# Optimization experiments

Hardware: AMD Instinct MI355X
Metric: run time of the kernel (lower is better)

The kernel has to match this reference:

```python
import jax, jax.numpy as jnp
import numpy as np

B, S, T = 512, 1024, 48

def setup_inputs() -> dict:
    key = jax.random.key(0)
    k1, k2, k3, k4, k5 = jax.random.split(key, 5)
    emissions = jax.random.normal(k1, (B, S, T), dtype=jnp.float32)
    tags = jax.random.randint(k2, (B, S), 0, T, dtype=jnp.int32)
    mask = jnp.ones((B, S), dtype=jnp.float32)
    transitions = jax.random.normal(k3, (T, T), dtype=jnp.float32)
    start_transitions = jax.random.normal(k4, (T,), dtype=jnp.float32)
    end_transitions = jax.random.normal(k5, (T,), dtype=jnp.float32)
    return {"emissions": emissions, "tags": tags, "mask": mask,
            "transitions": transitions, "start_transitions": start_transitions,
            "end_transitions": end_transitions}

def _crf_loss(emissions, transitions, start_transitions, end_transitions, tags, mask):
    # ---- numerator: score of the gold path (fully vectorized over seq) ----
    emit = jnp.take_along_axis(emissions, tags[..., None], axis=2)[..., 0]  # (B,S)
    trans = transitions[tags[:, 1:], tags[:, :-1]]                          # (B,S-1)
    lengths = jnp.sum(mask, axis=1).astype(jnp.int32)
    last_idx = jnp.clip(lengths - 1, 0)
    last_tags = jnp.take_along_axis(tags, last_idx[:, None], axis=1)[:, 0]
    numerator = (start_transitions[tags[:, 0]] + emit[:, 0]
                 + jnp.sum(mask[:, 1:] * (emit[:, 1:] + trans), axis=1)
                 + end_transitions[last_tags])                               # (B,)

    # ---- denominator: log-partition via forward algorithm (lax.scan) ----
    def step(score, x):
        em_i, m_i = x  # (B,T), (B,)
        # logsumexp over previous tag; emission is prev-independent so add outside
        nxt = jax.nn.logsumexp(score[:, :, None] + transitions.T[None, :, :], axis=1) + em_i
        score = jnp.where(m_i[:, None] > 0, nxt, score)
        return score, None

    init = start_transitions[None, :] + emissions[:, 0]                      # (B,T)
    xs = (jnp.swapaxes(emissions[:, 1:], 0, 1), jnp.swapaxes(mask[:, 1:], 0, 1))
    final, _ = jax.lax.scan(step, init, xs)
    denominator = jax.nn.logsumexp(final + end_transitions[None, :], axis=1)  # (B,)

    return jnp.mean(denominator - numerator)

def reference(emissions, tags, mask, transitions, start_transitions, end_transitions):
    return _crf_loss(emissions, transitions, start_transitions, end_transitions, tags, mask)
```

## Files before the change

kernel.cpp:

```cpp
#include <hip/hip_runtime.h>
#include <math.h>

#define Bn 512
#define Sn 1024
#define Tn 48
#define NSEG 16
#define SEGLEN 64

typedef _Float16 h2 __attribute__((ext_vector_type(2)));
typedef _Float16 h4 __attribute__((ext_vector_type(4)));
typedef float    f4 __attribute__((ext_vector_type(4)));

static constexpr float LOG2E = 1.4426950408889634f;
static constexpr float LN2f  = 0.6931471805599453f;

#define MFMA16(A, B, C) __builtin_amdgcn_mfma_f32_16x16x16f16((A), (B), (C), 0, 0, 0)

__device__ __forceinline__ h2 hmax2(h2 a, h2 b) {
#if __has_builtin(__builtin_elementwise_max)
  return __builtin_elementwise_max(a, b);
#else
  h2 r;
  r[0] = a[0] > b[0] ? a[0] : b[0];
  r[1] = a[1] > b[1] ? a[1] : b[1];
  return r;
#endif
}
__device__ __forceinline__ h2 cvt2(float a, float b) {
  return __builtin_bit_cast(h2, __builtin_amdgcn_cvt_pkrtz(a, b));
}
__device__ __forceinline__ h4 mkh4(h2 lo, h2 hi) {
  return __builtin_shufflevector(lo, hi, 0, 1, 2, 3);
}
__device__ __forceinline__ h2 loh(h4 v) { return __builtin_shufflevector(v, v, 0, 1); }
__device__ __forceinline__ h2 hih(h4 v) { return __builtin_shufflevector(v, v, 2, 3); }

__global__ __launch_bounds__(256) void ehgen(const float* __restrict__ em,
                                             _Float16* __restrict__ out) {
  const size_t total = (size_t)Bn * Sn * Tn;
  const size_t i = ((size_t)blockIdx.x * 256 + threadIdx.x) * 8;
  if (i >= total) return;
  const f4 a = *(const f4*)(em + i);
  const f4 b = *(const f4*)(em + i + 4);
  h4 o1, o2;
  #pragma unroll
  for (int j = 0; j < 4; ++j) {
    o1[j] = (_Float16)__builtin_amdgcn_exp2f(fmaf(a[j], LOG2E, -6.0f));
    o2[j] = (_Float16)__builtin_amdgcn_exp2f(fmaf(b[j], LOG2E, -6.0f));
  }
  *(h4*)(out + i) = o1;
  *(h4*)(out + i + 4) = o2;
}

template <bool PRE>
__global__ __launch_bounds__(1024, 2)
void crf_fwd_seg(const float* __restrict__ em,
                 const float* __restrict__ mask,
                 const float* __restrict__ trans,
                 const float* __restrict__ startt,
                 const float* __restrict__ endt,
                 const _Float16* __restrict__ eh16,
                 float* __restrict__ den_out)
{
  const int b   = blockIdx.x;
  const int tid = threadIdx.x;
  const int wid = tid >> 6;
  const int l   = tid & 63;
  const int c16 = l & 15;
  const int g   = l >> 4;

  __shared__ float lwbuf[64];

  const float*    __restrict__ emb = em + (size_t)b * Sn * Tn;
  const float*    __restrict__ mkb = mask + (size_t)b * Sn;
  const _Float16* __restrict__ ehL = PRE ? (eh16 + (size_t)b * Sn * Tn + 4 * g) : nullptr;
  const float*    __restrict__ emL = emb + 4 * g;

  h4 Afr[3][3];
  float mtg;
  {
    float tl[3][3][4];
    float mt = -1e30f;
    #pragma unroll
    for (int rt = 0; rt < 3; ++rt)
      #pragma unroll
      for (int kt = 0; kt < 3; ++kt) {
        const f4 t4 = *(const f4*)(trans + (16 * rt + c16) * Tn + 16 * kt + 4 * g);
        #pragma unroll
        for (int i = 0; i < 4; ++i) {
          const float v = t4[i] * LOG2E;
          tl[rt][kt][i] = v;
          mt = fmaxf(mt, v);
        }
      }
    #pragma unroll
    for (int off = 1; off < 64; off <<= 1) mt = fmaxf(mt, __shfl_xor(mt, off));
    mtg = mt;
    #pragma unroll
    for (int rt = 0; rt < 3; ++rt)
      #pragma unroll
      for (int kt = 0; kt < 3; ++kt) {
        h4 r;
        #pragma unroll
        for (int i = 0; i < 4; ++i)
          r[i] = (_Float16)__builtin_amdgcn_exp2f(tl[rt][kt][i] - mtg);
        Afr[rt][kt] = r;
      }
  }

  h4 Bfr[3][3];
  float Mc[3] = {0.f, 0.f, 0.f};
  float cnt = 0.f;
  #pragma unroll
  for (int kt = 0; kt < 3; ++kt)
    #pragma unroll
    for (int ct = 0; ct < 3; ++ct) {
      h4 r;
      #pragma unroll
      for (int i = 0; i < 4; ++i)
        r[i] = (_Float16)(((16 * kt + 4 * g + i) == (16 * ct + c16)) ? 1.0f : 0.0f);
      Bfr[kt][ct] = r;
    }

  auto STEP = [&](const h4& e0, const h4& e1, const h4& e2, float mkval,
                  bool APPLY, const float (&scv)[3], const float (&shv)[3]) {
    if (__int_as_float(__builtin_amdgcn_readfirstlane(__float_as_int(mkval))) > 0.0f) {
      f4 acc[3][3];
      #pragma unroll
      for (int rt = 0; rt < 3; ++rt)
        #pragma unroll
        for (int ct = 0; ct < 3; ++ct) acc[rt][ct] = f4{0.f, 0.f, 0.f, 0.f};
      #pragma unroll
      for (int kt = 0; kt < 3; ++kt)
        #pragma unroll
        for (int rt = 0; rt < 3; ++rt)
          #pragma unroll
          for (int ct = 0; ct < 3; ++ct)
            acc[rt][ct] = MFMA16(Afr[rt][kt], Bfr[kt][ct], acc[rt][ct]);
      const h4 ehv[3] = {e0, e1, e2};
      #pragma unroll
      for (int rt = 0; rt < 3; ++rt) {
        const h2 elo = loh(ehv[rt]);
        const h2 ehi = hih(ehv[rt]);
        #pragma unroll
        for (int ct = 0; ct < 3; ++ct) {
          f4 a = acc[rt][ct];
          if (APPLY) {
            a[0] *= scv[ct]; a[1] *= scv[ct]; a[2] *= scv[ct]; a[3] *= scv[ct];
          }
          const h2 lo = cvt2(a[0], a[1]) * elo;
          const h2 hi = cvt2(a[2], a[3]) * ehi;
          Bfr[rt][ct] = mkh4(lo, hi);
        }
      }
      if (APPLY) { Mc[0] += shv[0]; Mc[1] += shv[1]; Mc[2] += shv[2]; }
      cnt += 1.0f;
    }
  };

  auto MEASURE = [&](float (&sh)[3], float (&sc)[3]) {
    #pragma unroll
    for (int ct = 0; ct < 3; ++ct) {
      h2 m = loh(Bfr[0][ct]);
      m = hmax2(m, hih(Bfr[0][ct]));
      m = hmax2(m, loh(Bfr[1][ct]));
      m = hmax2(m, hih(Bfr[1][ct]));
      m = hmax2(m, loh(Bfr[2][ct]));
      m = hmax2(m, hih(Bfr[2][ct]));
      m = hmax2(m, __builtin_bit_cast(h2, __shfl_xor(__builtin_bit_cast(int, m), 16)));
      m = hmax2(m, __builtin_bit_cast(h2, __shfl_xor(__builtin_bit_cast(int, m), 32)));
      const float mf = fmaxf((float)m[0], (float)m[1]);
      int eb = ((__float_as_int(mf) >> 23) & 0xff) - 127;
      eb = eb < -15 ? -15 : (eb > 15 ? 15 : eb);
      sh[ct] = (float)eb;
      sc[ct] = __int_as_float((127 - eb) << 23);
    }
  };

  auto loadEH = [&](int s, h4& x, h4& y, h4& z) {
    if constexpr (PRE) {
      const _Float16* p = ehL + (size_t)s * Tn;
      x = *(const h4*)(p);
      y = *(const h4*)(p + 16);
      z = *(const h4*)(p + 32);
    } else {
      const float* p = emL + (size_t)s * Tn;
      const f4 a = *(const f4*)(p);
      const f4 b2 = *(const f4*)(p + 16);
      const f4 c2 = *(const f4*)(p + 32);
      f4 ea, eb2, ec;
      #pragma unroll
      for (int i = 0; i < 4; ++i) {
        ea[i]  = __builtin_amdgcn_exp2f(fmaf(a[i],  LOG2E, -6.0f));
        eb2[i] = __builtin_amdgcn_exp2f(fmaf(b2[i], LOG2E, -6.0f));
        ec[i]  = __builtin_amdgcn_exp2f(fmaf(c2[i], LOG2E, -6.0f));
      }
      x = mkh4(cvt2(ea[0], ea[1]), cvt2(ea[2], ea[3]));
      y = mkh4(cvt2(eb2[0], eb2[1]), cvt2(eb2[2], eb2[3]));
      z = mkh4(cvt2(ec[0], ec[1]), cvt2(ec[2], ec[3]));
    }
  };

  const int s_begin = 1 + SEGLEN * wid;
  const int nchunk  = (wid == NSEG - 1) ? 15 : 16;
  float shP[3] = {0.f, 0.f, 0.f}, scP[3] = {1.f, 1.f, 1.f};
  float shA[3] = {0.f, 0.f, 0.f}, scA[3] = {1.f, 1.f, 1.f};
  const float sh1[3] = {0.f, 0.f, 0.f};
  const float sc1[3] = {1.f, 1.f, 1.f};

  h4 E0, E1, E2, N0, N1, N2;
  f4 mkc = *(const f4*)(mkb + s_begin);
  f4 mkn;
  loadEH(s_begin, E0, E1, E2);
  int s = s_begin;
  #pragma unroll 1
  for (int c = 0; c < nchunk; ++c) {
    mkn = *(const f4*)(mkb + ((c + 1 < nchunk) ? (s + 4) : s));
    loadEH(s + 1, N0, N1, N2);
    STEP(E0, E1, E2, mkc[0], false, sc1, sh1);
    loadEH(s + 2, E0, E1, E2);
    STEP(N0, N1, N2, mkc[1], true, scP, shP);
    MEASURE(shA, scA);
    loadEH(s + 3, N0, N1, N2);
    STEP(E0, E1, E2, mkc[2], false, sc1, sh1);
    loadEH(s + 4, E0, E1, E2);
    STEP(N0, N1, N2, mkc[3], true, scA, shA);
    MEASURE(shP, scP);
    mkc = mkn;
    s += 4;
  }
  if (wid == NSEG - 1) {
    loadEH(1022, N0, N1, N2);
    STEP(E0, E1, E2, mkb[1021], false, sc1, sh1);
    loadEH(1023, E0, E1, E2);
    STEP(N0, N1, N2, mkb[1022], true, scP, shP);
    MEASURE(shA, scA);
    STEP(E0, E1, E2, mkb[1023], false, sc1, sh1);
  }

  const float addc = (mtg + 6.0f) * cnt;
  if (wid == 0 && l < Tn) lwbuf[l] = (startt[l] + emb[l]) * LOG2E;
  __syncthreads();
  #pragma unroll 1
  for (int sg = 0; sg < NSEG; ++sg) {
    if (wid == sg) {
      const float u0 = lwbuf[c16]      + Mc[0] + addc;
      const float u1 = lwbuf[16 + c16] + Mc[1] + addc;
      const float u2 = lwbuf[32 + c16] + Mc[2] + addc;
      float um = fmaxf(u0, fmaxf(u1, u2));
      #pragma unroll
      for (int off = 1; off < 64; off <<= 1) um = fmaxf(um, __shfl_xor(um, off));
      const float p0 = __builtin_amdgcn_exp2f(u0 - um);
      const float p1 = __builtin_amdgcn_exp2f(u1 - um);
      const float p2 = __builtin_amdgcn_exp2f(u2 - um);
      float rs[3][4];
      #pragma unroll
      for (int kt = 0; kt < 3; ++kt)
        #pragma unroll
        for (int i = 0; i < 4; ++i) {
          float v = (float)Bfr[kt][0][i] * p0;
          v = fmaf((float)Bfr[kt][1][i], p1, v);
          v = fmaf((float)Bfr[kt][2][i], p2, v);
          #pragma unroll
          for (int off = 1; off < 16; off <<= 1) v += __shfl_xor(v, off);
          rs[kt][i] = v;
        }
      if (c16 == 0) {
        #pragma unroll
        for (int kt = 0; kt < 3; ++kt)
          #pragma unroll
          for (int i = 0; i < 4; ++i)
            lwbuf[16 * kt + 4 * g + i] = um + __builtin_amdgcn_logf(rs[kt][i]);
      }
    }
    __syncthreads();
  }

  if (wid == 0) {
    float v = (l < Tn) ? lwbuf[l] + endt[l] * LOG2E : -INFINITY;
    float mv = v;
    #pragma unroll
    for (int off = 32; off; off >>= 1) mv = fmaxf(mv, __shfl_xor(mv, off));
    float zz = (l < Tn) ? __builtin_amdgcn_exp2f(v - mv) : 0.f;
    #pragma unroll
    for (int off = 32; off; off >>= 1) zz += __shfl_xor(zz, off);
    if (l == 0) den_out[b] = (mv + __builtin_amdgcn_logf(zz)) * LN2f;
  }
}

__global__ __launch_bounds__(256) void crf_numer(
    const float* __restrict__ em, const int* __restrict__ tags,
    const float* __restrict__ mask, const float* __restrict__ trans,
    const float* __restrict__ startt, const float* __restrict__ endt,
    float* __restrict__ num_out)
{
  const int b = blockIdx.x, t = threadIdx.x;
  const int*   tgb = tags + (size_t)b * Sn;
  const float* mkb = mask + (size_t)b * Sn;
  const float* emb = em + (size_t)b * Sn * Tn;

  const int s0 = t * 4;
  const int4 tg = *(const int4*)(tgb + s0);
  const f4   mk = *(const f4*)(mkb + s0);
  const int  tprev = (t == 0) ? 0 : tgb[s0 - 1];
  const int  tgarr[5] = {tprev, tg.x, tg.y, tg.z, tg.w};

  float acc  = 0.0f;
  float msum = mk[0] + mk[1] + mk[2] + mk[3];
  #pragma unroll
  for (int i = 0; i < 4; ++i) {
    const int s = s0 + i;
    if (s >= 1)
      acc += mk[i] * (emb[(size_t)s * Tn + tgarr[i + 1]] +
                      trans[tgarr[i + 1] * Tn + tgarr[i]]);
  }
  #pragma unroll
  for (int off = 32; off; off >>= 1) {
    acc  += __shfl_xor(acc, off);
    msum += __shfl_xor(msum, off);
  }
  __shared__ float ra[4], rm[4];
  if ((t & 63) == 0) { ra[t >> 6] = acc; rm[t >> 6] = msum; }
  __syncthreads();
  if (t == 0) {
    const float a = ra[0] + ra[1] + ra[2] + ra[3];
    const float m = rm[0] + rm[1] + rm[2] + rm[3];
    int last = (int)(m + 0.5f) - 1;
    if (last < 0) last = 0;
    const int lt = tgb[last];
    const int t0 = tgb[0];
    num_out[b] = startt[t0] + emb[t0] + a + endt[lt];
  }
}

__global__ __launch_bounds__(512) void reduce_loss(const float* __restrict__ den,
                                                   const float* __restrict__ num,
                                                   float* __restrict__ out) {
  __shared__ float red[8];
  const int t = threadIdx.x;
  float v = den[t] - num[t];
  #pragma unroll
  for (int off = 32; off; off >>= 1) v += __shfl_xor(v, off);
  if ((t & 63) == 0) red[t >> 6] = v;
  __syncthreads();
  if (t == 0) {
    float s = 0.f;
    #pragma unroll
    for (int wv = 0; wv < 8; ++wv) s += red[wv];
    out[0] = s * (1.0f / 512.0f);
  }
}

extern "C" void kernel_launch(void* const* d_in, const int* in_sizes, int n_in,
                              void* d_out, int out_size, void* d_ws, size_t ws_size,
                              hipStream_t stream) {
  const float* emissions = (const float*)d_in[0];
  const int*   tags      = (const int*)d_in[1];
  const float* mask      = (const float*)d_in[2];
  const float* trans     = (const float*)d_in[3];
  const float* startt    = (const float*)d_in[4];
  const float* endt      = (const float*)d_in[5];
  float* den_ws = (float*)d_ws;
  float* num_ws = den_ws + Bn;
  const size_t ehoff   = 4096;
  const size_t ehbytes = (size_t)Bn * Sn * Tn * sizeof(_Float16);
  _Float16* eh16 = (_Float16*)((char*)d_ws + ehoff);
  const bool pre = (ws_size >= ehoff + ehbytes);

  crf_numer<<<Bn, 256, 0, stream>>>(emissions, tags, mask, trans, startt, endt, num_ws);
  if (pre) {
    const int total8 = Bn * Sn * Tn / 8;
    ehgen<<<(total8 + 255) / 256, 256, 0, stream>>>(emissions, eh16);
    crf_fwd_seg<true><<<Bn, 1024, 0, stream>>>(emissions, mask, trans, startt, endt,
                                               eh16, den_ws);
  } else {
    crf_fwd_seg<false><<<Bn, 1024, 0, stream>>>(emissions, mask, trans, startt, endt,
                                                nullptr, den_ws);
  }
  reduce_loss<<<1, 512, 0, stream>>>(den_ws, num_ws, (float*)d_out);
}
```

Baseline: 227.6 us.

## Split each wave's segment into two interleaved independent chains for MFMA ILP

```diff
diff --git a/kernel.cpp b/kernel.cpp
--- a/kernel.cpp
+++ b/kernel.cpp
@@ -4,8 +4,8 @@
 #define Bn 512
 #define Sn 1024
 #define Tn 48
-#define NSEG 16
-#define SEGLEN 64
+#define NSEG 32
+#define SEGLEN 32
 
 typedef _Float16 h2 __attribute__((ext_vector_type(2)));
 typedef _Float16 h4 __attribute__((ext_vector_type(4)));
@@ -108,9 +108,9 @@
       }
   }
 
-  h4 Bfr[3][3];
-  float Mc[3] = {0.f, 0.f, 0.f};
-  float cnt = 0.f;
+  h4 BfA[3][3], BfB[3][3];
+  float McA[3] = {0.f, 0.f, 0.f}, McB[3] = {0.f, 0.f, 0.f};
+  float cntA = 0.f, cntB = 0.f;
   #pragma unroll
   for (int kt = 0; kt < 3; ++kt)
     #pragma unroll
@@ -119,63 +119,9 @@
       #pragma unroll
       for (int i = 0; i < 4; ++i)
         r[i] = (_Float16)(((16 * kt + 4 * g + i) == (16 * ct + c16)) ? 1.0f : 0.0f);
-      Bfr[kt][ct] = r;
-    }
-
-  auto STEP = [&](const h4& e0, const h4& e1, const h4& e2, float mkval,
-                  bool APPLY, const float (&scv)[3], const float (&shv)[3]) {
-    if (__int_as_float(__builtin_amdgcn_readfirstlane(__float_as_int(mkval))) > 0.0f) {
-      f4 acc[3][3];
-      #pragma unroll
-      for (int rt = 0; rt < 3; ++rt)
-        #pragma unroll
-        for (int ct = 0; ct < 3; ++ct) acc[rt][ct] = f4{0.f, 0.f, 0.f, 0.f};
-      #pragma unroll
-      for (int kt = 0; kt < 3; ++kt)
-        #pragma unroll
-        for (int rt = 0; rt < 3; ++rt)
-          #pragma unroll
-          for (int ct = 0; ct < 3; ++ct)
-            acc[rt][ct] = MFMA16(Afr[rt][kt], Bfr[kt][ct], acc[rt][ct]);
-      const h4 ehv[3] = {e0, e1, e2};
-      #pragma unroll
-      for (int rt = 0; rt < 3; ++rt) {
-        const h2 elo = loh(ehv[rt]);
-        const h2 ehi = hih(ehv[rt]);
-        #pragma unroll
-        for (int ct = 0; ct < 3; ++ct) {
-          f4 a = acc[rt][ct];
-          if (APPLY) {
-            a[0] *= scv[ct]; a[1] *= scv[ct]; a[2] *= scv[ct]; a[3] *= scv[ct];
-          }
-          const h2 lo = cvt2(a[0], a[1]) * elo;
-          const h2 hi = cvt2(a[2], a[3]) * ehi;
-          Bfr[rt][ct] = mkh4(lo, hi);
-        }
-      }
-      if (APPLY) { Mc[0] += shv[0]; Mc[1] += shv[1]; Mc[2] += shv[2]; }
-      cnt += 1.0f;
-    }
-  };
-
-  auto MEASURE = [&](float (&sh)[3], float (&sc)[3]) {
-    #pragma unroll
-    for (int ct = 0; ct < 3; ++ct) {
-      h2 m = loh(Bfr[0][ct]);
-      m = hmax2(m, hih(Bfr[0][ct]));
-      m = hmax2(m, loh(Bfr[1][ct]));
-      m = hmax2(m, hih(Bfr[1][ct]));
-      m = hmax2(m, loh(Bfr[2][ct]));
-      m = hmax2(m, hih(Bfr[2][ct]));
-      m = hmax2(m, __builtin_bit_cast(h2, __shfl_xor(__builtin_bit_cast(int, m), 16)));
-      m = hmax2(m, __builtin_bit_cast(h2, __shfl_xor(__builtin_bit_cast(int, m), 32)));
-      const float mf = fmaxf((float)m[0], (float)m[1]);
-      int eb = ((__float_as_int(mf) >> 23) & 0xff) - 127;
-      eb = eb < -15 ? -15 : (eb > 15 ? 15 : eb);
-      sh[ct] = (float)eb;
-      sc[ct] = __int_as_float((127 - eb) << 23);
-    }
-  };
+      BfA[kt][ct] = r;
+      BfB[kt][ct] = r;
+    }
 
   auto loadEH = [&](int s, h4& x, h4& y, h4& z) {
     if constexpr (PRE) {
@@ -201,77 +147,136 @@
     }
   };
 
-  const int s_begin = 1 + SEGLEN * wid;
-  const int nchunk  = (wid == NSEG - 1) ? 15 : 16;
-  float shP[3] = {0.f, 0.f, 0.f}, scP[3] = {1.f, 1.f, 1.f};
-  float shA[3] = {0.f, 0.f, 0.f}, scA[3] = {1.f, 1.f, 1.f};
-  const float sh1[3] = {0.f, 0.f, 0.f};
-  const float sc1[3] = {1.f, 1.f, 1.f};
-
-  h4 E0, E1, E2, N0, N1, N2;
-  f4 mkc = *(const f4*)(mkb + s_begin);
-  f4 mkn;
-  loadEH(s_begin, E0, E1, E2);
-  int s = s_begin;
+  auto STEP = [&](auto& Bf, auto& Mc, float& cnt, int s, bool APPLY,
+                  const float (&shv)[3]) {
+    const float mkval = mkb[s];
+    h4 e0, e1, e2;
+    loadEH(s, e0, e1, e2);
+    if (__int_as_float(__builtin_amdgcn_readfirstlane(__float_as_int(mkval))) > 0.0f) {
+      f4 acc[3][3];
+      #pragma unroll
+      for (int rt = 0; rt < 3; ++rt)
+        #pragma unroll
+        for (int ct = 0; ct < 3; ++ct) acc[rt][ct] = f4{0.f, 0.f, 0.f, 0.f};
+      #pragma unroll
+      for (int kt = 0; kt < 3; ++kt)
+        #pragma unroll
+        for (int rt = 0; rt < 3; ++rt)
+          #pragma unroll
+          for (int ct = 0; ct < 3; ++ct)
+            acc[rt][ct] = MFMA16(Afr[rt][kt], Bf[kt][ct], acc[rt][ct]);
+      float scv[3];
+      if (APPLY) {
+        #pragma unroll
+        for (int ct = 0; ct < 3; ++ct)
+          scv[ct] = __int_as_float((127 - (int)shv[ct]) << 23);
+      }
+      const h4 ehv[3] = {e0, e1, e2};
+      #pragma unroll
+      for (int rt = 0; rt < 3; ++rt) {
+        const h2 elo = loh(ehv[rt]);
+        const h2 ehi = hih(ehv[rt]);
+        #pragma unroll
+        for (int ct = 0; ct < 3; ++ct) {
+          f4 a = acc[rt][ct];
+          if (APPLY) {
+            a[0] *= scv[ct]; a[1] *= scv[ct]; a[2] *= scv[ct]; a[3] *= scv[ct];
+          }
+          const h2 lo = cvt2(a[0], a[1]) * elo;
+          const h2 hi = cvt2(a[2], a[3]) * ehi;
+          Bf[rt][ct] = mkh4(lo, hi);
+        }
+      }
+      if (APPLY) { Mc[0] += shv[0]; Mc[1] += shv[1]; Mc[2] += shv[2]; }
+      cnt += 1.0f;
+    }
+  };
+
+  auto MEASURE = [&](auto& Bf, float (&sh)[3]) {
+    #pragma unroll
+    for (int ct = 0; ct < 3; ++ct) {
+      h2 m = loh(Bf[0][ct]);
+      m = hmax2(m, hih(Bf[0][ct]));
+      m = hmax2(m, loh(Bf[1][ct]));
+      m = hmax2(m, hih(Bf[1][ct]));
+      m = hmax2(m, loh(Bf[2][ct]));
+      m = hmax2(m, hih(Bf[2][ct]));
+      m = hmax2(m, __builtin_bit_cast(h2, __shfl_xor(__builtin_bit_cast(int, m), 16)));
+      m = hmax2(m, __builtin_bit_cast(h2, __shfl_xor(__builtin_bit_cast(int, m), 32)));
+      const float mf = fmaxf((float)m[0], (float)m[1]);
+      int eb = ((__float_as_int(mf) >> 23) & 0xff) - 127;
+      eb = eb < -15 ? -15 : (eb > 15 ? 15 : eb);
+      sh[ct] = (float)eb;
+    }
+  };
+
+  float shPA[3] = {0.f, 0.f, 0.f}, shAA[3] = {0.f, 0.f, 0.f};
+  float shPB[3] = {0.f, 0.f, 0.f}, shAB[3] = {0.f, 0.f, 0.f};
+  int a = 1 + 2 * SEGLEN * wid;
+  int bs = a + SEGLEN;
   #pragma unroll 1
-  for (int c = 0; c < nchunk; ++c) {
-    mkn = *(const f4*)(mkb + ((c + 1 < nchunk) ? (s + 4) : s));
-    loadEH(s + 1, N0, N1, N2);
-    STEP(E0, E1, E2, mkc[0], false, sc1, sh1);
-    loadEH(s + 2, E0, E1, E2);
-    STEP(N0, N1, N2, mkc[1], true, scP, shP);
-    MEASURE(shA, scA);
-    loadEH(s + 3, N0, N1, N2);
-    STEP(E0, E1, E2, mkc[2], false, sc1, sh1);
-    loadEH(s + 4, E0, E1, E2);
-    STEP(N0, N1, N2, mkc[3], true, scA, shA);
-    MEASURE(shP, scP);
-    mkc = mkn;
-    s += 4;
-  }
-  if (wid == NSEG - 1) {
-    loadEH(1022, N0, N1, N2);
-    STEP(E0, E1, E2, mkb[1021], false, sc1, sh1);
-    loadEH(1023, E0, E1, E2);
-    STEP(N0, N1, N2, mkb[1022], true, scP, shP);
-    MEASURE(shA, scA);
-    STEP(E0, E1, E2, mkb[1023], false, sc1, sh1);
-  }
-
-  const float addc = (mtg + 6.0f) * cnt;
+  for (int c = 0; c < 7; ++c) {
+    STEP(BfA, McA, cntA, a + 0, false, shPA);
+    STEP(BfB, McB, cntB, bs + 0, false, shPB);
+    STEP(BfA, McA, cntA, a + 1, true,  shPA);  MEASURE(BfA, shAA);
+    STEP(BfB, McB, cntB, bs + 1, true,  shPB); MEASURE(BfB, shAB);
+    STEP(BfA, McA, cntA, a + 2, false, shPA);
+    STEP(BfB, McB, cntB, bs + 2, false, shPB);
+    STEP(BfA, McA, cntA, a + 3, true,  shAA);  MEASURE(BfA, shPA);
+    STEP(BfB, McB, cntB, bs + 3, true,  shAB); MEASURE(BfB, shPB);
+    a += 4; bs += 4;
+  }
+  STEP(BfA, McA, cntA, a + 0, false, shPA);
+  if (bs + 0 < Sn) STEP(BfB, McB, cntB, bs + 0, false, shPB);
+  STEP(BfA, McA, cntA, a + 1, true, shPA);  MEASURE(BfA, shAA);
+  if (bs + 1 < Sn) { STEP(BfB, McB, cntB, bs + 1, true, shPB); MEASURE(BfB, shAB); }
+  STEP(BfA, McA, cntA, a + 2, false, shPA);
+  if (bs + 2 < Sn) STEP(BfB, McB, cntB, bs + 2, false, shPB);
+  STEP(BfA, McA, cntA, a + 3, true, shAA);
+  if (bs + 3 < Sn) STEP(BfB, McB, cntB, bs + 3, true, shAB);
+
+  const float addcA = (mtg + 6.0f) * cntA;
+  const float addcB = (mtg + 6.0f) * cntB;
   if (wid == 0 && l < Tn) lwbuf[l] = (startt[l] + emb[l]) * LOG2E;
   __syncthreads();
+
+  auto APPLYM = [&](auto& Bf, auto& Mc, float addc) {
+    const float u0 = lwbuf[c16]      + Mc[0] + addc;
+    const float u1 = lwbuf[16 + c16] + Mc[1] + addc;
+    const float u2 = lwbuf[32 + c16] + Mc[2] + addc;
+    float um = fmaxf(u0, fmaxf(u1, u2));
+    #pragma unroll
+    for (int off = 1; off < 64; off <<= 1) um = fmaxf(um, __shfl_xor(um, off));
+    const float p0 = __builtin_amdgcn_exp2f(u0 - um);
+    const float p1 = __builtin_amdgcn_exp2f(u1 - um);
+    const float p2 = __builtin_amdgcn_exp2f(u2 - um);
+    float rs[3][4];
+    #pragma unroll
+    for (int kt = 0; kt < 3; ++kt)
+      #pragma unroll
+      for (int i = 0; i < 4; ++i) {
+        float v = (float)Bf[kt][0][i] * p0;
+        v = fmaf((float)Bf[kt][1][i], p1, v);
+        v = fmaf((float)Bf[kt][2][i], p2, v);
+        #pragma unroll
+        for (int off = 1; off < 16; off <<= 1) v += __shfl_xor(v, off);
+        rs[kt][i] = v;
+      }
+    if (c16 == 0) {
+      #pragma unroll
+      for (int kt = 0; kt < 3; ++kt)
+        #pragma unroll
+        for (int i = 0; i < 4; ++i)
+          lwbuf[16 * kt + 4 * g + i] = um + __builtin_amdgcn_logf(rs[kt][i]);
+    }
+  };
+
   #pragma unroll 1
-  for (int sg = 0; sg < NSEG; ++sg) {
-    if (wid == sg) {
-      const float u0 = lwbuf[c16]      + Mc[0] + addc;
-      const float u1 = lwbuf[16 + c16] + Mc[1] + addc;
-      const float u2 = lwbuf[32 + c16] + Mc[2] + addc;
-      float um = fmaxf(u0, fmaxf(u1, u2));
-      #pragma unroll
-      for (int off = 1; off < 64; off <<= 1) um = fmaxf(um, __shfl_xor(um, off));
-      const float p0 = __builtin_amdgcn_exp2f(u0 - um);
-      const float p1 = __builtin_amdgcn_exp2f(u1 - um);
-      const float p2 = __builtin_amdgcn_exp2f(u2 - um);
-      float rs[3][4];
-      #pragma unroll
-      for (int kt = 0; kt < 3; ++kt)
-        #pragma unroll
-        for (int i = 0; i < 4; ++i) {
-          float v = (float)Bfr[kt][0][i] * p0;
-          v = fmaf((float)Bfr[kt][1][i], p1, v);
-          v = fmaf((float)Bfr[kt][2][i], p2, v);
-          #pragma unroll
-          for (int off = 1; off < 16; off <<= 1) v += __shfl_xor(v, off);
-          rs[kt][i] = v;
-        }
-      if (c16 == 0) {
-        #pragma unroll
-        for (int kt = 0; kt < 3; ++kt)
-          #pragma unroll
-          for (int i = 0; i < 4; ++i)
-            lwbuf[16 * kt + 4 * g + i] = um + __builtin_amdgcn_logf(rs[kt][i]);
-      }
+  for (int t = 0; t < NSEG; ++t) {
+    if ((t & 1) == 0) {
+      if (wid == (t >> 1)) APPLYM(BfA, McA, addcA);
+    } else {
+      if (wid == (t >> 1)) APPLYM(BfB, McB, addcB);
     }
     __syncthreads();
   }
```

Measured after the change: 300.3 us. 1.32x slower.
